# Kernel tuning notes

Measured on AMD Instinct MI355X. Metric: run time of the kernel, lower is better.

The kernel has to match this reference:

```python
import jax, jax.numpy as jnp
import numpy as np
import math

B, T, E = 2, 2048, 2048
G, QPG, D = 4, 4, 128  # kv groups, queries per group, head dim (G*QPG*D == E)


def sinusoidal_pe(t, d, dtype):
    pos = jnp.arange(t, dtype=jnp.float32)[:, None]            # [T,1]
    i = jnp.arange(0, d, 2, dtype=jnp.float32)                 # [D/2]
    inv_freq = jnp.exp(-(jnp.log(10000.0) * i / d))            # [D/2]
    ang = pos * inv_freq                                       # [T,D/2]
    pe = jnp.zeros((t, d), dtype=jnp.float32)
    pe = pe.at[:, 0::2].set(jnp.sin(ang)).at[:, 1::2].set(jnp.cos(ang))
    return pe.astype(dtype)


def setup_inputs() -> dict:
    key = jax.random.key(0)
    ks = jax.random.split(key, 6)
    s = lambda fan_in: 1.0 / math.sqrt(fan_in)
    return {
        "x":   jax.random.normal(ks[0], (B, T, E), dtype=jnp.float32),
        "wq":  jax.random.uniform(ks[1], (E, G * QPG * D), jnp.float32, -s(E), s(E)),
        "bq":  jax.random.uniform(ks[2], (G * QPG * D,), jnp.float32, -s(E), s(E)),
        "wkv": jax.random.uniform(ks[3], (E, 2 * G * D), jnp.float32, -s(E), s(E)),
        "bkv": jax.random.uniform(ks[4], (2 * G * D,), jnp.float32, -s(E), s(E)),
        "wo":  jax.random.uniform(ks[5], (G * QPG * D, E), jnp.float32, -s(G * QPG * D), s(G * QPG * D)),
    }


def reference(x, wq, bq, wkv, bkv, wo):
    b, t, e = x.shape
    # projections
    q = (x @ wq + bq).reshape(b, t, G, QPG, D).transpose(0, 2, 3, 1, 4)   # [B,G,QPG,T,D]
    kv = (x @ wkv + bkv).reshape(b, t, G, 1, 2 * D).transpose(0, 2, 3, 1, 4)  # [B,G,1,T,2D]
    k, v = kv[..., :D], kv[..., D:]                                       # [B,G,1,T,D]
    # inline additive sinusoidal positional embedding on q and k
    pe = sinusoidal_pe(t, D, x.dtype)                                     # [T,D]
    q = q + pe
    k = k + pe
    # scores: [B,G,QPG,T,T] (kv head axis k has size 1, summed out)
    scores = jnp.einsum('bgqtd,bgksd->bgqts', q, k) / math.sqrt(D)
    causal = jnp.tril(jnp.ones((t, t), dtype=bool))                       # [T,T]
    scores = jnp.where(causal, scores, -jnp.inf)
    probs = jax.nn.softmax(scores, axis=-1)
    out = jnp.einsum('bgqts,bgksd->btgqd', probs, v).reshape(b, t, G * QPG * D)
    return out @ wo
```

## Files before the change

kernel.cpp:

```cpp
#include <hip/hip_runtime.h>
#include <stdint.h>

typedef __bf16 bf16;
typedef __bf16 bf16x4 __attribute__((ext_vector_type(4)));
typedef __bf16 bf16x8 __attribute__((ext_vector_type(8)));
typedef float floatx4 __attribute__((ext_vector_type(4)));

#define B_   2
#define T_   2048
#define E_   2048
#define G_   4
#define QPG_ 4
#define D_   128
#define H_   16
#define NQ   2048
#define NKV  1024
#define NQKV 3072
#define M_   4096

__device__ __forceinline__ void gload_lds16(const void* g, void* l) {
  __builtin_amdgcn_global_load_lds(
      (__attribute__((address_space(1))) unsigned int*)g,
      (__attribute__((address_space(3))) unsigned int*)l,
      16, 0, 0);
}

__device__ __forceinline__ int swz_stage_col(int lane) {
  return (((lane & 3) ^ ((lane >> 2) & 3) ^ ((lane >> 4) & 3))) * 8;
}


__global__ void cast_f32_bf16(const float* __restrict__ in, bf16* __restrict__ out, int n4) {
  int i = blockIdx.x * blockDim.x + threadIdx.x;
  if (i < n4) {
    float4 v = ((const float4*)in)[i];
    bf16x4 o = {(bf16)v.x, (bf16)v.y, (bf16)v.z, (bf16)v.w};
    ((bf16x4*)out)[i] = o;
  }
}

__global__ void transpose_cast(const float* __restrict__ in, bf16* __restrict__ out,
                               int R, int C, int out_stride) {
  __shared__ float tile[64][65];
  int r0 = blockIdx.x * 64, c0 = blockIdx.y * 64;
  int tx = threadIdx.x & 63, ty = threadIdx.x >> 6;
  for (int i = ty; i < 64; i += 4)
    tile[i][tx] = in[(size_t)(r0 + i) * C + c0 + tx];
  __syncthreads();
  for (int i = ty; i < 64; i += 4)
    out[(size_t)(c0 + i) * out_stride + r0 + tx] = (bf16)tile[tx][i];
}

__global__ void concat_bias(const float* __restrict__ bq, const float* __restrict__ bkv,
                            float* __restrict__ out) {
  int i = blockIdx.x * 256 + threadIdx.x;
  out[i] = (i < NQ) ? bq[i] : bkv[i - NQ];
}


template <int OUT_BF16, int HAS_BIAS>
__global__ __launch_bounds__(256, 2) void gemm_bt(
    const bf16* __restrict__ A, const bf16* __restrict__ Bt,
    const float* __restrict__ bias, void* __restrict__ Cout,
    int M, int N, int K) {
  __shared__ __align__(16) bf16 As[128 * 32];
  __shared__ __align__(16) bf16 Bs[128 * 32];
  const int tid = threadIdx.x;
  const int wave = tid >> 6, lane = tid & 63;
  const int quad = lane >> 4, c = lane & 15;
  const int m0 = blockIdx.x * 128, n0 = blockIdx.y * 128;
  const int wr = (wave >> 1) * 64, wc = (wave & 1) * 64;
  const int xsl = ((quad ^ (c & 3) ^ ((c >> 2) & 3)) & 3) * 8;

  floatx4 acc[4][4];
#pragma unroll
  for (int i = 0; i < 4; ++i)
#pragma unroll
    for (int j = 0; j < 4; ++j) acc[i][j] = (floatx4){0.f, 0.f, 0.f, 0.f};

  const int srow = wave * 32 + (lane >> 2);
  const int scol = swz_stage_col(lane);
  const bf16* Ap = A + (size_t)(m0 + srow) * K + scol;
  const bf16* Bp = Bt + (size_t)(n0 + srow) * K + scol;

  for (int k0 = 0; k0 < K; k0 += 32) {
#pragma unroll
    for (int ch = 0; ch < 2; ++ch) {
      gload_lds16(Ap + (size_t)ch * 16 * K + k0, &As[(wave * 2 + ch) * 512]);
      gload_lds16(Bp + (size_t)ch * 16 * K + k0, &Bs[(wave * 2 + ch) * 512]);
    }
    __syncthreads();
    bf16x8 af[4], bfr[4];
#pragma unroll
    for (int i = 0; i < 4; ++i) {
      af[i]  = *(const bf16x8*)(&As[(wr + i * 16 + c) * 32 + xsl]);
      bfr[i] = *(const bf16x8*)(&Bs[(wc + i * 16 + c) * 32 + xsl]);
    }
#pragma unroll
    for (int mi = 0; mi < 4; ++mi)
#pragma unroll
      for (int ni = 0; ni < 4; ++ni)
        acc[mi][ni] = __builtin_amdgcn_mfma_f32_16x16x32_bf16(af[mi], bfr[ni], acc[mi][ni], 0, 0, 0);
    __syncthreads();
  }

  float bv[4] = {0.f, 0.f, 0.f, 0.f};
  if (HAS_BIAS) {
#pragma unroll
    for (int ni = 0; ni < 4; ++ni) bv[ni] = bias[n0 + wc + ni * 16 + c];
  }
#pragma unroll
  for (int mi = 0; mi < 4; ++mi) {
#pragma unroll
    for (int ni = 0; ni < 4; ++ni) {
      const int col = n0 + wc + ni * 16 + c;
#pragma unroll
      for (int r = 0; r < 4; ++r) {
        const int row = m0 + wr + mi * 16 + quad * 4 + r;
        float v = acc[mi][ni][r] + bv[ni];
        if (OUT_BF16)
          ((bf16*)Cout)[(size_t)row * N + col] = (bf16)v;
        else
          ((float*)Cout)[(size_t)row * N + col] = v;
      }
    }
  }
}


__device__ __forceinline__ float pe_val(int t, int d) {
  int i2 = d & ~1;
  float inv = __expf(-9.210340371976184f * (float)i2 * (1.0f / 128.0f));
  float ang = (float)t * inv;
  return (d & 1) ? cosf(ang) : sinf(ang);
}

__global__ void scatter_qk(const bf16* __restrict__ qkv,
                           bf16* __restrict__ Qb, bf16* __restrict__ Kb) {
  const int row = blockIdx.x;
  const int b = row >> 11, t = row & 2047;
  const int tid = threadIdx.x;
  const int d = tid & 127;
  const float scale = 0.12751745f;
  const float pe = pe_val(t, d);
  for (int h = tid >> 7; h < H_; h += 2) {
    float q = (float)qkv[(size_t)row * NQKV + h * 128 + d] + pe;
    Qb[((size_t)(b * H_ + h) * T_ + t) * D_ + d] = (bf16)(q * scale);
  }
  for (int g = tid >> 7; g < G_; g += 2) {
    float k = (float)qkv[(size_t)row * NQKV + NQ + g * 256 + d] + pe;
    Kb[((size_t)(b * G_ + g) * T_ + t) * D_ + d] = (bf16)k;
  }
}

__global__ void build_vt(const bf16* __restrict__ qkv, bf16* __restrict__ Vt) {
  __shared__ float tile[64][65];
  int t0 = blockIdx.x * 64, d0 = blockIdx.y * 64;
  int bg = blockIdx.z, b = bg >> 2, g = bg & 3;
  const bf16* src = qkv + (size_t)b * T_ * NQKV + NQ + g * 256 + 128;
  bf16* dst = Vt + (size_t)bg * D_ * T_;
  int tx = threadIdx.x & 63, ty = threadIdx.x >> 6;
  for (int i = ty; i < 64; i += 4)
    tile[i][tx] = (float)src[(size_t)(t0 + i) * NQKV + d0 + tx];
  __syncthreads();
  for (int i = ty; i < 64; i += 4)
    dst[(size_t)(d0 + i) * T_ + t0 + tx] = (bf16)tile[tx][i];
}


__global__ __launch_bounds__(512, 4) void flash_attn(
    const bf16* __restrict__ Qb, const bf16* __restrict__ Kb,
    const bf16* __restrict__ Vt, bf16* __restrict__ Ob) {
  const int i = blockIdx.x;
  const int qt = 31 - (i >> 5);
  const int bh = i & 31;
  const int b = bh >> 4, h = bh & 15, g2 = h >> 2;
  const int tid = threadIdx.x;
  const int wave = tid >> 6, lane = tid & 63;
  const int grp = wave >> 2, w4 = wave & 3;
  const int quad = lane >> 4, c = lane & 15;
  const int xsl = ((quad ^ (c & 3) ^ ((c >> 2) & 3)) & 3) * 8;

  __shared__ __align__(16) char smem[75776];
  bf16* Ks = (bf16*)smem;
  bf16* Vs = (bf16*)(smem + 32768);
  bf16* Pq = (bf16*)(smem + 65536);

  const int q0 = qt * 64;
  const bf16* Qbase = Qb + ((size_t)(b * H_ + h) * T_ + q0 + w4 * 16 + c) * D_;
  bf16x8 qf[4];
#pragma unroll
  for (int ks = 0; ks < 4; ++ks)
    qf[ks] = *(const bf16x8*)(Qbase + ks * 32 + quad * 8);

  floatx4 acc[8];
#pragma unroll
  for (int nd = 0; nd < 8; ++nd) acc[nd] = (floatx4){0.f, 0.f, 0.f, 0.f};
  float rsum[4] = {0.f, 0.f, 0.f, 0.f};

  const bf16* Kg = Kb + (size_t)(b * G_ + g2) * T_ * D_;
  const bf16* Vg = Vt + (size_t)(b * G_ + g2) * D_ * T_;
  const int slr = lane >> 2;
  const int slc = swz_stage_col(lane);
  const int ng = qt + 1;
  const int jbase = grp * ng;
  const int amax = 2 * qt + (w4 >> 1);

  auto stage = [&](int t, int bu) {
    const int k0 = t * 32;
    bf16* kd = Ks + ((grp * 2 + bu) * 4 + w4) * 1024;
    bf16* vd = Vs + ((grp * 2 + bu) * 4 + w4) * 1024;
#pragma unroll
    for (int hh = 0; hh < 2; ++hh) {
      gload_lds16(Kg + (size_t)(k0 + hh * 16 + slr) * D_ + w4 * 32 + slc, kd + hh * 512);
      gload_lds16(Vg + (size_t)(w4 * 32 + hh * 16 + slr) * T_ + k0 + slc, vd + hh * 512);
    }
  };

  stage(jbase, 0);

  for (int jg = 0; jg < ng; ++jg) {
    __syncthreads();
    if (jg + 1 < ng) stage(jbase + jg + 1, (jg + 1) & 1);
    const int j = jbase + jg;
    if (j > amax) continue;

    const bf16* Kt  = Ks + (grp * 2 + (jg & 1)) * 4096;
    const bf16* Vtl = Vs + (grp * 2 + (jg & 1)) * 4096;

    floatx4 s[2];
    s[0] = (floatx4){0.f, 0.f, 0.f, 0.f};
    s[1] = (floatx4){0.f, 0.f, 0.f, 0.f};
#pragma unroll
    for (int ks = 0; ks < 4; ++ks)
#pragma unroll
      for (int n = 0; n < 2; ++n) {
        bf16x8 kf = *(const bf16x8*)(Kt + ks * 1024 + (n * 16 + c) * 32 + xsl);
        s[n] = __builtin_amdgcn_mfma_f32_16x16x32_bf16(qf[ks], kf, s[n], 0, 0, 0);
      }

    if (j == amax) {
      const int colb = j * 32;
      const int rowb = q0 + w4 * 16 + quad * 4;
#pragma unroll
      for (int n = 0; n < 2; ++n)
#pragma unroll
        for (int r = 0; r < 4; ++r)
          if (colb + n * 16 + c > rowb + r) s[n][r] = -1e30f;
    }

    bf16* Pw = Pq + wave * 640;
#pragma unroll
    for (int n = 0; n < 2; ++n)
#pragma unroll
      for (int r = 0; r < 4; ++r) {
        float p = exp2f(s[n][r]);
        rsum[r] += p;
        Pw[(quad * 4 + r) * 40 + n * 16 + c] = (bf16)p;
      }

    bf16x8 pf = *(const bf16x8*)(&Pw[c * 40 + quad * 8]);

#pragma unroll
    for (int nd = 0; nd < 8; ++nd) {
      bf16x8 vf = *(const bf16x8*)(Vtl + (nd >> 1) * 1024 + ((nd & 1) * 16 + c) * 32 + xsl);
      acc[nd] = __builtin_amdgcn_mfma_f32_16x16x32_bf16(pf, vf, acc[nd], 0, 0, 0);
    }
  }

#pragma unroll
  for (int off = 1; off < 16; off <<= 1)
#pragma unroll
    for (int r = 0; r < 4; ++r) rsum[r] += __shfl_xor(rsum[r], off);

  __syncthreads();
  float* mrg = (float*)smem;
  float* mrs = (float*)(smem + 34816);
  const int row16 = w4 * 16 + quad * 4;

  if (grp == 0) {
#pragma unroll
    for (int nd2 = 0; nd2 < 4; ++nd2)
#pragma unroll
      for (int r = 0; r < 4; ++r)
        mrg[(row16 + r) * 68 + nd2 * 16 + c] = acc[4 + nd2][r];
  } else {
#pragma unroll
    for (int nd2 = 0; nd2 < 4; ++nd2)
#pragma unroll
      for (int r = 0; r < 4; ++r)
        mrg[(64 + row16 + r) * 68 + nd2 * 16 + c] = acc[nd2][r];
  }
  if (c == 0) {
#pragma unroll
    for (int r = 0; r < 4; ++r) mrs[grp * 64 + row16 + r] = rsum[r];
  }
  __syncthreads();

  const int og = grp ^ 1;
  float linv[4];
#pragma unroll
  for (int r = 0; r < 4; ++r) linv[r] = 1.f / (rsum[r] + mrs[og * 64 + row16 + r]);

  if (grp == 0) {
#pragma unroll
    for (int nd2 = 0; nd2 < 4; ++nd2)
#pragma unroll
      for (int r = 0; r < 4; ++r) {
        float o = acc[nd2][r] + mrg[(64 + row16 + r) * 68 + nd2 * 16 + c];
        const int trow = q0 + row16 + r;
        Ob[((size_t)(b * T_ + trow)) * NQ + h * D_ + nd2 * 16 + c] = (bf16)(o * linv[r]);
      }
  } else {
#pragma unroll
    for (int nd2 = 0; nd2 < 4; ++nd2)
#pragma unroll
      for (int r = 0; r < 4; ++r) {
        float o = acc[4 + nd2][r] + mrg[(row16 + r) * 68 + nd2 * 16 + c];
        const int trow = q0 + row16 + r;
        Ob[((size_t)(b * T_ + trow)) * NQ + h * D_ + (4 + nd2) * 16 + c] = (bf16)(o * linv[r]);
      }
  }
}


extern "C" void kernel_launch(void* const* d_in, const int* in_sizes, int n_in,
                              void* d_out, int out_size, void* d_ws, size_t ws_size,
                              hipStream_t stream) {
  const float* x   = (const float*)d_in[0];
  const float* wq  = (const float*)d_in[1];
  const float* bq  = (const float*)d_in[2];
  const float* wkv = (const float*)d_in[3];
  const float* bkv = (const float*)d_in[4];
  const float* wo  = (const float*)d_in[5];
  float* out = (float*)d_out;

  char* p = (char*)d_ws;
  bf16* xb    = (bf16*)p; p += (size_t)M_ * E_ * 2;
  bf16* wqkvT = (bf16*)p; p += (size_t)NQKV * E_ * 2;
  bf16* woT   = (bf16*)p; p += (size_t)E_ * NQ * 2;
  float* biasq = (float*)p; p += 16384;
  bf16* qkv   = (bf16*)p; p += (size_t)M_ * NQKV * 2;
  bf16* Qb    = (bf16*)p; p += (size_t)B_ * H_ * T_ * D_ * 2;
  bf16* Kb    = (bf16*)p; p += (size_t)B_ * G_ * T_ * D_ * 2;
  bf16* Vtb   = (bf16*)p; p += (size_t)B_ * G_ * D_ * T_ * 2;
  bf16* Ob    = (bf16*)p; p += (size_t)M_ * NQ * 2;

  cast_f32_bf16<<<(M_ * E_ / 4) / 256, 256, 0, stream>>>(x, xb, M_ * E_ / 4);
  transpose_cast<<<dim3(E_ / 64, E_ / 64), 256, 0, stream>>>(wq, wqkvT, E_, E_, E_);
  transpose_cast<<<dim3(E_ / 64, NKV / 64), 256, 0, stream>>>(wkv, wqkvT + (size_t)NQ * E_, E_, NKV, E_);
  transpose_cast<<<dim3(E_ / 64, E_ / 64), 256, 0, stream>>>(wo, woT, NQ, E_, NQ);
  concat_bias<<<NQKV / 256, 256, 0, stream>>>(bq, bkv, biasq);

  gemm_bt<1, 1><<<dim3(M_ / 128, NQKV / 128), 256, 0, stream>>>(xb, wqkvT, biasq, qkv, M_, NQKV, E_);
  scatter_qk<<<M_, 256, 0, stream>>>(qkv, Qb, Kb);
  build_vt<<<dim3(T_ / 64, D_ / 64, B_ * G_), 256, 0, stream>>>(qkv, Vtb);
  flash_attn<<<1024, 512, 0, stream>>>(Qb, Kb, Vtb, Ob);
  gemm_bt<0, 0><<<dim3(M_ / 128, E_ / 128), 256, 0, stream>>>(Ob, woT, nullptr, out, M_, E_, NQ);
}
```

Baseline: 325.0 us.

## Double flash-attention query tile to 128 rows per block for K/V reuse

Each wave now computes two 16-row query sub-tiles against the same K/V fragments. This halves the grid and the K/V staging traffic per query row. The tile-to-block mapping is reordered to balance causal work, and the P scratch writes and reads in LDS get an XOR swizzle to cut bank conflicts. The cost is twice the accumulator and Q registers per wave under the existing launch bounds, which risks spills or lower occupancy, and fewer blocks to spread the causal imbalance.

```diff
diff --git a/kernel.cpp b/kernel.cpp
--- a/kernel.cpp
+++ b/kernel.cpp
@@ -172,8 +172,8 @@
     const bf16* __restrict__ Qb, const bf16* __restrict__ Kb,
     const bf16* __restrict__ Vt, bf16* __restrict__ Ob) {
   const int i = blockIdx.x;
-  const int qt = 31 - (i >> 5);
-  const int bh = i & 31;
+  const int tpos = i >> 5, bh = i & 31;
+  const int t = (tpos < 8) ? tpos : 23 - tpos;
   const int b = bh >> 4, h = bh & 15, g2 = h >> 2;
   const int tid = threadIdx.x;
   const int wave = tid >> 6, lane = tid & 63;
@@ -186,28 +186,33 @@
   bf16* Vs = (bf16*)(smem + 32768);
   bf16* Pq = (bf16*)(smem + 65536);
 
-  const int q0 = qt * 64;
-  const bf16* Qbase = Qb + ((size_t)(b * H_ + h) * T_ + q0 + w4 * 16 + c) * D_;
-  bf16x8 qf[4];
-#pragma unroll
-  for (int ks = 0; ks < 4; ++ks)
-    qf[ks] = *(const bf16x8*)(Qbase + ks * 32 + quad * 8);
-
-  floatx4 acc[8];
-#pragma unroll
-  for (int nd = 0; nd < 8; ++nd) acc[nd] = (floatx4){0.f, 0.f, 0.f, 0.f};
-  float rsum[4] = {0.f, 0.f, 0.f, 0.f};
+  const int q0 = t * 128;
+  bf16x8 qf[2][4];
+#pragma unroll
+  for (int hf = 0; hf < 2; ++hf) {
+    const bf16* Qbase = Qb + ((size_t)(b * H_ + h) * T_ + q0 + w4 * 32 + hf * 16 + c) * D_;
+#pragma unroll
+    for (int ks = 0; ks < 4; ++ks)
+      qf[hf][ks] = *(const bf16x8*)(Qbase + ks * 32 + quad * 8);
+  }
+
+  floatx4 acc[2][8];
+#pragma unroll
+  for (int hf = 0; hf < 2; ++hf)
+#pragma unroll
+    for (int nd = 0; nd < 8; ++nd) acc[hf][nd] = (floatx4){0.f, 0.f, 0.f, 0.f};
+  float rsum[2][4] = {{0.f, 0.f, 0.f, 0.f}, {0.f, 0.f, 0.f, 0.f}};
 
   const bf16* Kg = Kb + (size_t)(b * G_ + g2) * T_ * D_;
   const bf16* Vg = Vt + (size_t)(b * G_ + g2) * D_ * T_;
   const int slr = lane >> 2;
   const int slc = swz_stage_col(lane);
-  const int ng = qt + 1;
+  const int ng = 2 * (t + 1);
   const int jbase = grp * ng;
-  const int amax = 2 * qt + (w4 >> 1);
-
-  auto stage = [&](int t, int bu) {
-    const int k0 = t * 32;
+  const int amax = 4 * t + w4;
+
+  auto stage = [&](int tt, int bu) {
+    const int k0 = tt * 32;
     bf16* kd = Ks + ((grp * 2 + bu) * 4 + w4) * 1024;
     bf16* vd = Vs + ((grp * 2 + bu) * 4 + w4) * 1024;
 #pragma unroll
@@ -228,98 +233,120 @@
     const bf16* Kt  = Ks + (grp * 2 + (jg & 1)) * 4096;
     const bf16* Vtl = Vs + (grp * 2 + (jg & 1)) * 4096;
 
-    floatx4 s[2];
-    s[0] = (floatx4){0.f, 0.f, 0.f, 0.f};
-    s[1] = (floatx4){0.f, 0.f, 0.f, 0.f};
+    floatx4 s[2][2];
+#pragma unroll
+    for (int hf = 0; hf < 2; ++hf)
+#pragma unroll
+      for (int n = 0; n < 2; ++n) s[hf][n] = (floatx4){0.f, 0.f, 0.f, 0.f};
 #pragma unroll
     for (int ks = 0; ks < 4; ++ks)
 #pragma unroll
       for (int n = 0; n < 2; ++n) {
         bf16x8 kf = *(const bf16x8*)(Kt + ks * 1024 + (n * 16 + c) * 32 + xsl);
-        s[n] = __builtin_amdgcn_mfma_f32_16x16x32_bf16(qf[ks], kf, s[n], 0, 0, 0);
+        s[0][n] = __builtin_amdgcn_mfma_f32_16x16x32_bf16(qf[0][ks], kf, s[0][n], 0, 0, 0);
+        s[1][n] = __builtin_amdgcn_mfma_f32_16x16x32_bf16(qf[1][ks], kf, s[1][n], 0, 0, 0);
       }
 
     if (j == amax) {
       const int colb = j * 32;
-      const int rowb = q0 + w4 * 16 + quad * 4;
+#pragma unroll
+      for (int hf = 0; hf < 2; ++hf) {
+        const int rowb = q0 + w4 * 32 + hf * 16 + quad * 4;
+#pragma unroll
+        for (int n = 0; n < 2; ++n)
+#pragma unroll
+          for (int r = 0; r < 4; ++r)
+            if (colb + n * 16 + c > rowb + r) s[hf][n][r] = -1e30f;
+      }
+    }
+
+    bf16* Pw = Pq + wave * 640;
+    bf16x8 pf[2];
+#pragma unroll
+    for (int hf = 0; hf < 2; ++hf) {
 #pragma unroll
       for (int n = 0; n < 2; ++n)
 #pragma unroll
-        for (int r = 0; r < 4; ++r)
-          if (colb + n * 16 + c > rowb + r) s[n][r] = -1e30f;
-    }
-
-    bf16* Pw = Pq + wave * 640;
-#pragma unroll
-    for (int n = 0; n < 2; ++n)
-#pragma unroll
-      for (int r = 0; r < 4; ++r) {
-        float p = exp2f(s[n][r]);
-        rsum[r] += p;
-        Pw[(quad * 4 + r) * 40 + n * 16 + c] = (bf16)p;
-      }
-
-    bf16x8 pf = *(const bf16x8*)(&Pw[c * 40 + quad * 8]);
+        for (int r = 0; r < 4; ++r) {
+          float p = exp2f(s[hf][n][r]);
+          rsum[hf][r] += p;
+          const int chs = (n * 2 + (c >> 3)) ^ quad;
+          Pw[(quad * 4 + r) * 40 + chs * 8 + (c & 7)] = (bf16)p;
+        }
+      pf[hf] = *(const bf16x8*)(&Pw[c * 40 + ((quad ^ ((c >> 2) & 3))) * 8]);
+    }
 
 #pragma unroll
     for (int nd = 0; nd < 8; ++nd) {
       bf16x8 vf = *(const bf16x8*)(Vtl + (nd >> 1) * 1024 + ((nd & 1) * 16 + c) * 32 + xsl);
-      acc[nd] = __builtin_amdgcn_mfma_f32_16x16x32_bf16(pf, vf, acc[nd], 0, 0, 0);
+      acc[0][nd] = __builtin_amdgcn_mfma_f32_16x16x32_bf16(pf[0], vf, acc[0][nd], 0, 0, 0);
+      acc[1][nd] = __builtin_amdgcn_mfma_f32_16x16x32_bf16(pf[1], vf, acc[1][nd], 0, 0, 0);
     }
   }
 
 #pragma unroll
   for (int off = 1; off < 16; off <<= 1)
 #pragma unroll
-    for (int r = 0; r < 4; ++r) rsum[r] += __shfl_xor(rsum[r], off);
+    for (int hf = 0; hf < 2; ++hf)
+#pragma unroll
+      for (int r = 0; r < 4; ++r) rsum[hf][r] += __shfl_xor(rsum[hf][r], off);
 
   __syncthreads();
   float* mrg = (float*)smem;
-  float* mrs = (float*)(smem + 34816);
-  const int row16 = w4 * 16 + quad * 4;
+  float* mrs = (float*)(smem + 69632);
+  const int rw = w4 * 32 + quad * 4;
 
   if (grp == 0) {
 #pragma unroll
-    for (int nd2 = 0; nd2 < 4; ++nd2)
-#pragma unroll
-      for (int r = 0; r < 4; ++r)
-        mrg[(row16 + r) * 68 + nd2 * 16 + c] = acc[4 + nd2][r];
+    for (int hf = 0; hf < 2; ++hf)
+#pragma unroll
+      for (int nd2 = 0; nd2 < 4; ++nd2)
+#pragma unroll
+        for (int r = 0; r < 4; ++r)
+          mrg[(size_t)(rw + hf * 16 + r) * 68 + nd2 * 16 + c] = acc[hf][4 + nd2][r];
   } else {
 #pragma unroll
-    for (int nd2 = 0; nd2 < 4; ++nd2)
-#pragma unroll
-      for (int r = 0; r < 4; ++r)
-        mrg[(64 + row16 + r) * 68 + nd2 * 16 + c] = acc[nd2][r];
+    for (int hf = 0; hf < 2; ++hf)
+#pragma unroll
+      for (int nd2 = 0; nd2 < 4; ++nd2)
+#pragma unroll
+        for (int r = 0; r < 4; ++r)
+          mrg[(size_t)(128 + rw + hf * 16 + r) * 68 + nd2 * 16 + c] = acc[hf][nd2][r];
   }
   if (c == 0) {
 #pragma unroll
-    for (int r = 0; r < 4; ++r) mrs[grp * 64 + row16 + r] = rsum[r];
+    for (int hf = 0; hf < 2; ++hf)
+#pragma unroll
+      for (int r = 0; r < 4; ++r) mrs[grp * 128 + rw + hf * 16 + r] = rsum[hf][r];
   }
   __syncthreads();
 
   const int og = grp ^ 1;
-  float linv[4];
-#pragma unroll
-  for (int r = 0; r < 4; ++r) linv[r] = 1.f / (rsum[r] + mrs[og * 64 + row16 + r]);
-
-  if (grp == 0) {
-#pragma unroll
-    for (int nd2 = 0; nd2 < 4; ++nd2)
-#pragma unroll
-      for (int r = 0; r < 4; ++r) {
-        float o = acc[nd2][r] + mrg[(64 + row16 + r) * 68 + nd2 * 16 + c];
-        const int trow = q0 + row16 + r;
-        Ob[((size_t)(b * T_ + trow)) * NQ + h * D_ + nd2 * 16 + c] = (bf16)(o * linv[r]);
-      }
-  } else {
-#pragma unroll
-    for (int nd2 = 0; nd2 < 4; ++nd2)
-#pragma unroll
-      for (int r = 0; r < 4; ++r) {
-        float o = acc[4 + nd2][r] + mrg[(row16 + r) * 68 + nd2 * 16 + c];
-        const int trow = q0 + row16 + r;
-        Ob[((size_t)(b * T_ + trow)) * NQ + h * D_ + (4 + nd2) * 16 + c] = (bf16)(o * linv[r]);
-      }
+#pragma unroll
+  for (int hf = 0; hf < 2; ++hf) {
+    float linv[4];
+#pragma unroll
+    for (int r = 0; r < 4; ++r)
+      linv[r] = 1.f / (rsum[hf][r] + mrs[og * 128 + rw + hf * 16 + r]);
+    if (grp == 0) {
+#pragma unroll
+      for (int nd2 = 0; nd2 < 4; ++nd2)
+#pragma unroll
+        for (int r = 0; r < 4; ++r) {
+          float o = acc[hf][nd2][r] + mrg[(size_t)(128 + rw + hf * 16 + r) * 68 + nd2 * 16 + c];
+          const int trow = q0 + rw + hf * 16 + r;
+          Ob[((size_t)(b * T_ + trow)) * NQ + h * D_ + nd2 * 16 + c] = (bf16)(o * linv[r]);
+        }
+    } else {
+#pragma unroll
+      for (int nd2 = 0; nd2 < 4; ++nd2)
+#pragma unroll
+        for (int r = 0; r < 4; ++r) {
+          float o = acc[hf][4 + nd2][r] + mrg[(size_t)(rw + hf * 16 + r) * 68 + nd2 * 16 + c];
+          const int trow = q0 + rw + hf * 16 + r;
+          Ob[((size_t)(b * T_ + trow)) * NQ + h * D_ + (4 + nd2) * 16 + c] = (bf16)(o * linv[r]);
+        }
+    }
   }
 }
 
@@ -355,6 +382,6 @@
   gemm_bt<1, 1><<<dim3(M_ / 128, NQKV / 128), 256, 0, stream>>>(xb, wqkvT, biasq, qkv, M_, NQKV, E_);
   scatter_qk<<<M_, 256, 0, stream>>>(qkv, Qb, Kb);
   build_vt<<<dim3(T_ / 64, D_ / 64, B_ * G_), 256, 0, stream>>>(qkv, Vtb);
-  flash_attn<<<1024, 512, 0, stream>>>(Qb, Kb, Vtb, Ob);
+  flash_attn<<<512, 512, 0, stream>>>(Qb, Kb, Vtb, Ob);
   gemm_bt<0, 0><<<dim3(M_ / 128, E_ / 128), 256, 0, stream>>>(Ob, woT, nullptr, out, M_, E_, NQ);
 }
```

Result: slower. 364.9 us (+12.3%).
